# Kernel optimization log

Hardware: AMD Instinct MI355X
Metric: run time of the kernel (lower is better)

## Reference

```python
import jax, jax.numpy as jnp
import numpy as np
from jax import lax

B, C, H, W = 32, 64, 112, 112
ALPHA, BETA1, BETA2 = 0.25, 1.0, 1.0

# STE sign for weights (DifferntiableSign): fwd = +/-1, bwd mask |w|<=1 (w in [-1,1))
@jax.custom_vjp
def dsign(w):
    return jnp.where(w >= 0, 1.0, -1.0).astype(w.dtype)
def _dsign_fwd(w):
    return dsign(w), w
def _dsign_bwd(w, g):
    return (g * ((w < 1) & (w >= -1)).astype(g.dtype),)
dsign.defvjp(_dsign_fwd, _dsign_bwd)

# ReActNet BinaryActivation: fwd = sign(x), bwd piecewise-polynomial STE
@jax.custom_vjp
def bin_act(x):
    return jnp.where(x >= 0, 1.0, -1.0).astype(x.dtype)
def _ba_fwd(x):
    return bin_act(x), x
def _ba_bwd(x, g):
    slope = jnp.where((x >= -1) & (x < 0), 2.0 + 2.0 * x,
             jnp.where((x >= 0) & (x < 1), 2.0 - 2.0 * x, 0.0))
    return (g * slope.astype(g.dtype),)
bin_act.defvjp(_ba_fwd, _ba_bwd)

def scaled_sign_conv(x, w):
    # per-output-channel scale = mean(|w|) over (in, kh, kw)
    scale = jnp.mean(jnp.abs(w), axis=(1, 2, 3), keepdims=True)
    wb = scale * dsign(w)
    return lax.conv_general_dilated(x, wb, window_strides=(1, 1),
                                    padding=((1, 1), (1, 1)),
                                    dimension_numbers=("NCHW", "OIHW", "NCHW"))

def add_bias(x, b):
    return x + b[None, :, None, None]

def prelu(x, a):
    return jnp.where(x >= 0, x, a[None, :, None, None] * x)

def setup_inputs() -> dict:
    key = jax.random.key(0)
    ks = jax.random.split(key, 12)
    x = jax.random.normal(ks[0], (B, C, H, W), dtype=jnp.float32)
    # conv weights: symmetric uniform in [-1e-3, 1e-3] so signs are nontrivial
    w3 = (jax.random.uniform(ks[1], (C, C, 3, 3)) - 0.5) * 0.002
    w_pw = (jax.random.uniform(ks[2], (C, C, 3, 3)) - 0.5) * 0.002
    b11 = jax.random.normal(ks[3], (C,)) * 0.01
    b12 = jax.random.normal(ks[4], (C,)) * 0.01
    b13 = jax.random.normal(ks[5], (C,)) * 0.01
    b21 = jax.random.normal(ks[6], (C,)) * 0.01
    b22 = jax.random.normal(ks[7], (C,)) * 0.01
    b23 = jax.random.normal(ks[8], (C,)) * 0.01
    a1 = jax.random.uniform(ks[9], (C,), minval=0.1, maxval=0.4)
    a2 = jax.random.uniform(ks[10], (C,), minval=0.1, maxval=0.4)
    return {"x": x, "w3": w3, "w_pw": w_pw, "b11": b11, "b12": b12, "b13": b13,
            "b21": b21, "b22": b22, "b23": b23, "a1": a1, "a2": a2}

def reference(x, w3, w_pw, b11, b12, b13, b21, b22, b23, a1, a2):
    x_in = x * BETA1
    out1 = add_bias(x_in, b11)            # move11
    out1 = bin_act(out1)
    out1 = scaled_sign_conv(out1, w3)     # binary_3x3
    out1 = x + out1 * ALPHA               # stride==1: residual is original x
    out1 = add_bias(out1, b12)            # move12
    out1 = prelu(out1, a1)
    out1 = add_bias(out1, b13)            # move13
    out1_in = out1 * BETA2
    out2 = add_bias(out1_in, b21)         # move21
    out2 = bin_act(out2)
    out2 = scaled_sign_conv(out2, w_pw)   # binary_pw (3x3 per given defaults)
    out2 = out2 * ALPHA + out1
    out2 = add_bias(out2, b22)            # move22
    out2 = prelu(out2, a2)
    out2 = add_bias(out2, b23)            # move23
    return out2
```

## Files before the change

### kernel.cpp

```cpp
#include <hip/hip_runtime.h>
#include <hip/hip_fp16.h>
#include <stdint.h>

#define Bn 32
#define Cc 64
#define Hh 112
#define Ww 112
#define HWp (Hh*Ww)
#define NPIX (Bn*HWp)
#define PW 114
#define PHW (PW*PW)
#define NPAIR (HWp/2)
#define WROW (Ww/2)
#define ALPHA 0.25f
#define CSP 4
#define CPB (Cc/CSP)

typedef float    f32x2 __attribute__((ext_vector_type(2)));
typedef _Float16 f16x2 __attribute__((ext_vector_type(2)));

#define WB1_OFF   0
#define WB2_OFF   4608
#define ASC1_OFF  9216
#define ASC2_OFF  9472
#define CI1_OFF   9728
#define CI2_OFF   12288
#define BITS1_OFF 16384
#define BITS2_OFF (16384 + 3326976)
#define OUT1H_OFF (16384 + 2*3326976)
#define WS_NEED   (OUT1H_OFF + (size_t)NPIX*Cc*2)

#define MEMFENCE() asm volatile("" ::: "memory")

__global__ __launch_bounds__(64) void prep_weights(
        const float* __restrict__ w3, const float* __restrict__ wpw,
        uint64_t* __restrict__ wb1, uint64_t* __restrict__ wb2,
        float* __restrict__ asc1, float* __restrict__ asc2,
        int* __restrict__ ci1, int* __restrict__ ci2) {
    int b = blockIdx.x;
    int lane = threadIdx.x;
    const float* w  = (b < 64) ? w3   : wpw;
    uint64_t* wbits = (b < 64) ? wb1  : wb2;
    float*    ascp  = (b < 64) ? asc1 : asc2;
    int*      cip   = (b < 64) ? ci1  : ci2;
    int o = b & 63;
    const float* wp = w + ((size_t)o * Cc + lane) * 9;
    float v[9]; float asum = 0.f;
    #pragma unroll
    for (int t = 0; t < 9; ++t) { v[t] = wp[t]; asum += fabsf(v[t]); }
    uint64_t bal[9];
    #pragma unroll
    for (int t = 0; t < 9; ++t) bal[t] = __ballot(v[t] < 0.f);
    if (lane < 9) {
        wbits[o * 9 + lane] = bal[lane];
        int ty = lane, tr = ty / 3, tc = ty % 3;
        int sum = 0;
        #pragma unroll
        for (int t = 0; t < 9; ++t) {
            int r = t / 3, c = t % 3;
            bool inv = (tr == 0 && r == 0) || (tr == 2 && r == 2) ||
                       (tc == 0 && c == 0) || (tc == 2 && c == 2);
            if (inv) sum += 64 - 2 * (int)__popcll(bal[t]);
        }
        cip[o * 10 + ty] = 576 - sum;
    }
    #pragma unroll
    for (int off = 32; off > 0; off >>= 1) asum += __shfl_down(asum, off, 64);
    if (lane == 0) ascp[o] = ALPHA * asum * (1.f / 576.f);
}

__global__ __launch_bounds__(256, 4) void pack1(const float* __restrict__ x,
                                                const float* __restrict__ b11,
                                                uint64_t* __restrict__ bits1,
                                                uint64_t* __restrict__ bits2) {
    int n = blockIdx.y;
    int z = blockIdx.z;
    if (blockIdx.x >= 25) {
        if (z) return;
        int t = (blockIdx.x - 25) * 256 + threadIdx.x;
        if (t < 2 * PW + 2 * Hh) {
            int cell;
            if      (t < PW)          cell = t;
            else if (t < 2 * PW)      cell = 113 * PW + (t - PW);
            else if (t < 2 * PW + Hh) cell = (t - 2 * PW + 1) * PW;
            else                      cell = (t - 2 * PW - Hh + 1) * PW + 113;
            size_t bi = (size_t)n * PHW + cell;
            bits1[bi] = 0; bits2[bi] = 0;
        }
        return;
    }
    int p = blockIdx.x * 256 + threadIdx.x;
    if (p >= NPAIR) return;
    int h = p / WROW, w0 = (p - h * WROW) * 2;
    int hw = h * Ww + w0;
    int cb = z * 32;
    const float* xp = x + ((size_t)n * Cc + cb) * HWp + hw;
    size_t bi = (size_t)n * PHW + (h + 1) * PW + (w0 + 1);

    f32x2 v[32];
    #pragma unroll
    for (int j = 0; j < 32; ++j) v[j] = *(const f32x2*)(xp + (size_t)j * HWp);
    MEMFENCE();

    uint32_t ma = 0, mb = 0;
    #pragma unroll
    for (int j = 0; j < 32; ++j) {
        float bb = b11[cb + j];
        if (v[j].x + bb < 0.f) ma |= (1u << j);
        if (v[j].y + bb < 0.f) mb |= (1u << j);
    }
    uint32_t* wp1 = (uint32_t*)(bits1 + bi);
    wp1[z]     = ma;
    wp1[2 + z] = mb;
}

template <typename OutT>
__global__ __launch_bounds__(256, 4) void conv1_ep(
        const float* __restrict__ x, const uint64_t* __restrict__ bits1,
        const uint64_t* __restrict__ wb, const float* __restrict__ asc,
        const int* __restrict__ cint,
        const float* __restrict__ b12, const float* __restrict__ a1,
        const float* __restrict__ b13, const float* __restrict__ b21,
        OutT* __restrict__ out1, uint64_t* __restrict__ bits2) {
    __shared__ int lci[CPB * 10];
    int zb = blockIdx.z;
    int ob = zb * CPB;
    for (int i = threadIdx.x; i < CPB * 10; i += 256) lci[i] = cint[ob * 10 + i];
    __syncthreads();

    int p = blockIdx.x * 256 + threadIdx.x;
    if (p >= NPAIR) return;
    int n = blockIdx.y;
    int h = p / WROW, w0 = (p - h * WROW) * 2;
    int hw = h * Ww + w0;
    int rowp = (h == 0) ? 0 : (h == Hh - 1) ? 6 : 3;
    int t9a = rowp + ((w0 == 0) ? 0 : 1);
    int t9b = rowp + ((w0 + 1 == Ww - 1) ? 2 : 1);

    const uint64_t* bp = bits1 + (size_t)n * PHW + (h + 1) * PW + (w0 + 1);
    uint64_t q0[4], q1[4], q2[4];
    #pragma unroll
    for (int c = 0; c < 4; ++c) {
        q0[c] = bp[-PW - 1 + c]; q1[c] = bp[-1 + c]; q2[c] = bp[PW - 1 + c];
    }

    const float* xp = x + ((size_t)n * Cc + ob) * HWp + hw;
    OutT* op = out1 + ((size_t)n * Cc + ob) * HWp + hw;

    f32x2 cur[CPB];
    #pragma unroll
    for (int j = 0; j < CPB; ++j) cur[j] = *(const f32x2*)(xp + (size_t)j * HWp);
    MEMFENCE();

    uint32_t m2a = 0, m2b = 0;
    #pragma unroll
    for (int j = 0; j < CPB; ++j) {
        int o = ob + j;
        const uint64_t* wo = wb + o * 9;
        uint64_t t0 = wo[0], t1 = wo[1], t2 = wo[2], t3 = wo[3], t4 = wo[4],
                 t5 = wo[5], t6 = wo[6], t7 = wo[7], t8 = wo[8];
        int sa = (int)__popcll(q0[0] ^ t0) + (int)__popcll(q0[1] ^ t1) + (int)__popcll(q0[2] ^ t2)
               + (int)__popcll(q1[0] ^ t3) + (int)__popcll(q1[1] ^ t4) + (int)__popcll(q1[2] ^ t5)
               + (int)__popcll(q2[0] ^ t6) + (int)__popcll(q2[1] ^ t7) + (int)__popcll(q2[2] ^ t8);
        int sb = (int)__popcll(q0[1] ^ t0) + (int)__popcll(q0[2] ^ t1) + (int)__popcll(q0[3] ^ t2)
               + (int)__popcll(q1[1] ^ t3) + (int)__popcll(q1[2] ^ t4) + (int)__popcll(q1[3] ^ t5)
               + (int)__popcll(q2[1] ^ t6) + (int)__popcll(q2[2] ^ t7) + (int)__popcll(q2[3] ^ t8);
        int ca = lci[j * 10 + t9a];
        int cb = lci[j * 10 + t9b];
        float sc = asc[o], B2 = b12[o], Am1 = a1[o] - 1.0f, B3 = b13[o], B1 = b21[o];
        float va = fmaf(sc, (float)(ca - 2 * sa), cur[j].x);
        float vb = fmaf(sc, (float)(cb - 2 * sb), cur[j].y);
        va += B2; va = fmaf(fminf(va, 0.f), Am1, va); va += B3;
        vb += B2; vb = fmaf(fminf(vb, 0.f), Am1, vb); vb += B3;
        if constexpr (sizeof(OutT) == 2) {
            f16x2 hv; hv.x = (_Float16)va; hv.y = (_Float16)vb;
            *(f16x2*)(op + (size_t)j * HWp) = hv;
        } else {
            f32x2 fv; fv.x = va; fv.y = vb;
            *(f32x2*)(op + (size_t)j * HWp) = fv;
        }
        if (va + B1 < 0.f) m2a |= (1u << j);
        if (vb + B1 < 0.f) m2b |= (1u << j);
    }
    uint16_t* b2p = (uint16_t*)(bits2 + (size_t)n * PHW + (h + 1) * PW + (w0 + 1));
    b2p[zb]     = (uint16_t)m2a;
    b2p[4 + zb] = (uint16_t)m2b;
}

template <typename InT>
__global__ __launch_bounds__(256, 4) void conv2_ep(
        const uint64_t* __restrict__ bits2, const InT* __restrict__ out1,
        const uint64_t* __restrict__ wb, const float* __restrict__ asc,
        const int* __restrict__ cint,
        const float* __restrict__ b22, const float* __restrict__ a2,
        const float* __restrict__ b23, float* __restrict__ out) {
    __shared__ int lci[CPB * 10];
    int zb = blockIdx.z;
    int ob = zb * CPB;
    for (int i = threadIdx.x; i < CPB * 10; i += 256) lci[i] = cint[ob * 10 + i];
    __syncthreads();

    int p = blockIdx.x * 256 + threadIdx.x;
    if (p >= NPAIR) return;
    int n = blockIdx.y;
    int h = p / WROW, w0 = (p - h * WROW) * 2;
    int hw = h * Ww + w0;
    int rowp = (h == 0) ? 0 : (h == Hh - 1) ? 6 : 3;
    int t9a = rowp + ((w0 == 0) ? 0 : 1);
    int t9b = rowp + ((w0 + 1 == Ww - 1) ? 2 : 1);

    const uint64_t* bp = bits2 + (size_t)n * PHW + (h + 1) * PW + (w0 + 1);
    uint64_t q0[4], q1[4], q2[4];
    #pragma unroll
    for (int c = 0; c < 4; ++c) {
        q0[c] = bp[-PW - 1 + c]; q1[c] = bp[-1 + c]; q2[c] = bp[PW - 1 + c];
    }

    const InT* ip = out1 + ((size_t)n * Cc + ob) * HWp + hw;
    float* op = out + ((size_t)n * Cc + ob) * HWp + hw;

    f16x2 curh[CPB];
    f32x2 curf[CPB];
    if constexpr (sizeof(InT) == 2) {
        #pragma unroll
        for (int j = 0; j < CPB; ++j) curh[j] = *(const f16x2*)(ip + (size_t)j * HWp);
    } else {
        #pragma unroll
        for (int j = 0; j < CPB; ++j) curf[j] = *(const f32x2*)(ip + (size_t)j * HWp);
    }
    MEMFENCE();

    #pragma unroll
    for (int j = 0; j < CPB; ++j) {
        int o = ob + j;
        const uint64_t* wo = wb + o * 9;
        uint64_t t0 = wo[0], t1 = wo[1], t2 = wo[2], t3 = wo[3], t4 = wo[4],
                 t5 = wo[5], t6 = wo[6], t7 = wo[7], t8 = wo[8];
        int sa = (int)__popcll(q0[0] ^ t0) + (int)__popcll(q0[1] ^ t1) + (int)__popcll(q0[2] ^ t2)
               + (int)__popcll(q1[0] ^ t3) + (int)__popcll(q1[1] ^ t4) + (int)__popcll(q1[2] ^ t5)
               + (int)__popcll(q2[0] ^ t6) + (int)__popcll(q2[1] ^ t7) + (int)__popcll(q2[2] ^ t8);
        int sb = (int)__popcll(q0[1] ^ t0) + (int)__popcll(q0[2] ^ t1) + (int)__popcll(q0[3] ^ t2)
               + (int)__popcll(q1[1] ^ t3) + (int)__popcll(q1[2] ^ t4) + (int)__popcll(q1[3] ^ t5)
               + (int)__popcll(q2[1] ^ t6) + (int)__popcll(q2[2] ^ t7) + (int)__popcll(q2[3] ^ t8);
        int ca = lci[j * 10 + t9a];
        int cb = lci[j * 10 + t9b];
        float ra, rb;
        if constexpr (sizeof(InT) == 2) { ra = (float)curh[j].x; rb = (float)curh[j].y; }
        else                            { ra = curf[j].x;        rb = curf[j].y; }
        float sc = asc[o], B2 = b22[o], Am1 = a2[o] - 1.0f, B3 = b23[o];
        float va = fmaf(sc, (float)(ca - 2 * sa), ra);
        float vb = fmaf(sc, (float)(cb - 2 * sb), rb);
        va += B2; va = fmaf(fminf(va, 0.f), Am1, va); va += B3;
        vb += B2; vb = fmaf(fminf(vb, 0.f), Am1, vb); vb += B3;
        f32x2 fv; fv.x = va; fv.y = vb;
        __builtin_nontemporal_store(fv, (f32x2*)(op + (size_t)j * HWp));
    }
}

extern "C" void kernel_launch(void* const* d_in, const int* in_sizes, int n_in,
                              void* d_out, int out_size, void* d_ws, size_t ws_size,
                              hipStream_t stream) {
    const float* x    = (const float*)d_in[0];
    const float* w3   = (const float*)d_in[1];
    const float* wpw  = (const float*)d_in[2];
    const float* b11  = (const float*)d_in[3];
    const float* b12  = (const float*)d_in[4];
    const float* b13  = (const float*)d_in[5];
    const float* b21  = (const float*)d_in[6];
    const float* b22  = (const float*)d_in[7];
    const float* b23  = (const float*)d_in[8];
    const float* a1   = (const float*)d_in[9];
    const float* a2   = (const float*)d_in[10];

    char* ws = (char*)d_ws;
    uint64_t* wb1   = (uint64_t*)(ws + WB1_OFF);
    uint64_t* wb2   = (uint64_t*)(ws + WB2_OFF);
    float*    asc1  = (float*)(ws + ASC1_OFF);
    float*    asc2  = (float*)(ws + ASC2_OFF);
    int*      ci1   = (int*)(ws + CI1_OFF);
    int*      ci2   = (int*)(ws + CI2_OFF);
    uint64_t* bits1 = (uint64_t*)(ws + BITS1_OFF);
    uint64_t* bits2 = (uint64_t*)(ws + BITS2_OFF);
    float*    out   = (float*)d_out;

    dim3 pgrid(27, Bn, 2);
    dim3 cgrid((NPAIR + 255) / 256, Bn, CSP);

    prep_weights<<<128, 64, 0, stream>>>(w3, wpw, wb1, wb2, asc1, asc2, ci1, ci2);
    pack1<<<pgrid, 256, 0, stream>>>(x, b11, bits1, bits2);

    if (ws_size >= WS_NEED) {
        __half* out1h = (__half*)(ws + OUT1H_OFF);
        conv1_ep<__half><<<cgrid, 256, 0, stream>>>(x, bits1, wb1, asc1, ci1,
                                                    b12, a1, b13, b21, out1h, bits2);
        conv2_ep<__half><<<cgrid, 256, 0, stream>>>(bits2, out1h, wb2, asc2, ci2,
                                                    b22, a2, b23, out);
    } else {
        conv1_ep<float><<<cgrid, 256, 0, stream>>>(x, bits1, wb1, asc1, ci1,
                                                   b12, a1, b13, b21, out, bits2);
        conv2_ep<float><<<cgrid, 256, 0, stream>>>(bits2, out, wb2, asc2, ci2,
                                                   b22, a2, b23, out);
    }
}
```

Measured before the change: 272.2 us.

## Process four pixels per thread and split channels finer across blocks

Each thread in the pack and conv kernels now handles four adjacent pixels with 128-bit vector loads and stores instead of two. The channel split grows from 4 to 8 groups in the conv kernels and from 2 to 4 in the pack kernel, and the bit-mask writes shrink to 16-bit and 8-bit pieces. This reuses the loaded neighbour bit-words across more outputs and widens memory transactions, cutting redundant bit loads per pixel. In exchange each thread needs more registers, and the narrower partial writes into shared 64-bit words become finer-grained.

After: 271.6 us. No clear change (-0.2%).

```diff
diff --git a/kernel.cpp b/kernel.cpp
--- a/kernel.cpp
+++ b/kernel.cpp
@@ -10,14 +10,17 @@
 #define NPIX (Bn*HWp)
 #define PW 114
 #define PHW (PW*PW)
-#define NPAIR (HWp/2)
-#define WROW (Ww/2)
+#define NQUAD (HWp/4)
+#define QROW (Ww/4)
 #define ALPHA 0.25f
-#define CSP 4
-#define CPB (Cc/CSP)
+#define CSPC 8
+#define CPB (Cc/CSPC)
+#define PSP 4
 
 typedef float    f32x2 __attribute__((ext_vector_type(2)));
+typedef float    f32x4 __attribute__((ext_vector_type(4)));
 typedef _Float16 f16x2 __attribute__((ext_vector_type(2)));
+typedef _Float16 f16x4 __attribute__((ext_vector_type(4)));
 
 #define WB1_OFF   0
 #define WB2_OFF   4608
@@ -75,9 +78,9 @@
                                                 uint64_t* __restrict__ bits2) {
     int n = blockIdx.y;
     int z = blockIdx.z;
-    if (blockIdx.x >= 25) {
+    if (blockIdx.x >= 13) {
         if (z) return;
-        int t = (blockIdx.x - 25) * 256 + threadIdx.x;
+        int t = (blockIdx.x - 13) * 256 + threadIdx.x;
         if (t < 2 * PW + 2 * Hh) {
             int cell;
             if      (t < PW)          cell = t;
@@ -90,28 +93,33 @@
         return;
     }
     int p = blockIdx.x * 256 + threadIdx.x;
-    if (p >= NPAIR) return;
-    int h = p / WROW, w0 = (p - h * WROW) * 2;
+    if (p >= NQUAD) return;
+    int h = p / QROW, qx = p - h * QROW;
+    int w0 = qx * 4;
     int hw = h * Ww + w0;
-    int cb = z * 32;
+    int cb = z * 16;
     const float* xp = x + ((size_t)n * Cc + cb) * HWp + hw;
     size_t bi = (size_t)n * PHW + (h + 1) * PW + (w0 + 1);
 
-    f32x2 v[32];
-    #pragma unroll
-    for (int j = 0; j < 32; ++j) v[j] = *(const f32x2*)(xp + (size_t)j * HWp);
+    f32x4 v[16];
+    #pragma unroll
+    for (int j = 0; j < 16; ++j) v[j] = *(const f32x4*)(xp + (size_t)j * HWp);
     MEMFENCE();
 
-    uint32_t ma = 0, mb = 0;
-    #pragma unroll
-    for (int j = 0; j < 32; ++j) {
+    uint32_t ma = 0, mb = 0, mc = 0, md = 0;
+    #pragma unroll
+    for (int j = 0; j < 16; ++j) {
         float bb = b11[cb + j];
         if (v[j].x + bb < 0.f) ma |= (1u << j);
         if (v[j].y + bb < 0.f) mb |= (1u << j);
-    }
-    uint32_t* wp1 = (uint32_t*)(bits1 + bi);
-    wp1[z]     = ma;
-    wp1[2 + z] = mb;
+        if (v[j].z + bb < 0.f) mc |= (1u << j);
+        if (v[j].w + bb < 0.f) md |= (1u << j);
+    }
+    uint16_t* wp1 = (uint16_t*)(bits1 + bi);
+    wp1[z]      = (uint16_t)ma;
+    wp1[4 + z]  = (uint16_t)mb;
+    wp1[8 + z]  = (uint16_t)mc;
+    wp1[12 + z] = (uint16_t)md;
 }
 
 template <typename OutT>
@@ -129,30 +137,32 @@
     __syncthreads();
 
     int p = blockIdx.x * 256 + threadIdx.x;
-    if (p >= NPAIR) return;
+    if (p >= NQUAD) return;
     int n = blockIdx.y;
-    int h = p / WROW, w0 = (p - h * WROW) * 2;
+    int h = p / QROW, qx = p - h * QROW;
+    int w0 = qx * 4;
     int hw = h * Ww + w0;
     int rowp = (h == 0) ? 0 : (h == Hh - 1) ? 6 : 3;
-    int t9a = rowp + ((w0 == 0) ? 0 : 1);
-    int t9b = rowp + ((w0 + 1 == Ww - 1) ? 2 : 1);
+    int t9a = rowp + ((qx == 0) ? 0 : 1);
+    int t9m = rowp + 1;
+    int t9d = rowp + ((qx == QROW - 1) ? 2 : 1);
 
     const uint64_t* bp = bits1 + (size_t)n * PHW + (h + 1) * PW + (w0 + 1);
-    uint64_t q0[4], q1[4], q2[4];
-    #pragma unroll
-    for (int c = 0; c < 4; ++c) {
+    uint64_t q0[6], q1[6], q2[6];
+    #pragma unroll
+    for (int c = 0; c < 6; ++c) {
         q0[c] = bp[-PW - 1 + c]; q1[c] = bp[-1 + c]; q2[c] = bp[PW - 1 + c];
     }
 
     const float* xp = x + ((size_t)n * Cc + ob) * HWp + hw;
     OutT* op = out1 + ((size_t)n * Cc + ob) * HWp + hw;
 
-    f32x2 cur[CPB];
-    #pragma unroll
-    for (int j = 0; j < CPB; ++j) cur[j] = *(const f32x2*)(xp + (size_t)j * HWp);
+    f32x4 cur[CPB];
+    #pragma unroll
+    for (int j = 0; j < CPB; ++j) cur[j] = *(const f32x4*)(xp + (size_t)j * HWp);
     MEMFENCE();
 
-    uint32_t m2a = 0, m2b = 0;
+    uint32_t m2a = 0, m2b = 0, m2c = 0, m2d = 0;
     #pragma unroll
     for (int j = 0; j < CPB; ++j) {
         int o = ob + j;
@@ -165,26 +175,42 @@
         int sb = (int)__popcll(q0[1] ^ t0) + (int)__popcll(q0[2] ^ t1) + (int)__popcll(q0[3] ^ t2)
                + (int)__popcll(q1[1] ^ t3) + (int)__popcll(q1[2] ^ t4) + (int)__popcll(q1[3] ^ t5)
                + (int)__popcll(q2[1] ^ t6) + (int)__popcll(q2[2] ^ t7) + (int)__popcll(q2[3] ^ t8);
+        int sc_ = (int)__popcll(q0[2] ^ t0) + (int)__popcll(q0[3] ^ t1) + (int)__popcll(q0[4] ^ t2)
+               + (int)__popcll(q1[2] ^ t3) + (int)__popcll(q1[3] ^ t4) + (int)__popcll(q1[4] ^ t5)
+               + (int)__popcll(q2[2] ^ t6) + (int)__popcll(q2[3] ^ t7) + (int)__popcll(q2[4] ^ t8);
+        int sd = (int)__popcll(q0[3] ^ t0) + (int)__popcll(q0[4] ^ t1) + (int)__popcll(q0[5] ^ t2)
+               + (int)__popcll(q1[3] ^ t3) + (int)__popcll(q1[4] ^ t4) + (int)__popcll(q1[5] ^ t5)
+               + (int)__popcll(q2[3] ^ t6) + (int)__popcll(q2[4] ^ t7) + (int)__popcll(q2[5] ^ t8);
         int ca = lci[j * 10 + t9a];
-        int cb = lci[j * 10 + t9b];
-        float sc = asc[o], B2 = b12[o], Am1 = a1[o] - 1.0f, B3 = b13[o], B1 = b21[o];
-        float va = fmaf(sc, (float)(ca - 2 * sa), cur[j].x);
-        float vb = fmaf(sc, (float)(cb - 2 * sb), cur[j].y);
+        int cm = lci[j * 10 + t9m];
+        int cd = lci[j * 10 + t9d];
+        float scl = asc[o], B2 = b12[o], Am1 = a1[o] - 1.0f, B3 = b13[o], B1 = b21[o];
+        float va = fmaf(scl, (float)(ca - 2 * sa), cur[j].x);
+        float vb = fmaf(scl, (float)(cm - 2 * sb), cur[j].y);
+        float vc = fmaf(scl, (float)(cm - 2 * sc_), cur[j].z);
+        float vd = fmaf(scl, (float)(cd - 2 * sd), cur[j].w);
         va += B2; va = fmaf(fminf(va, 0.f), Am1, va); va += B3;
         vb += B2; vb = fmaf(fminf(vb, 0.f), Am1, vb); vb += B3;
+        vc += B2; vc = fmaf(fminf(vc, 0.f), Am1, vc); vc += B3;
+        vd += B2; vd = fmaf(fminf(vd, 0.f), Am1, vd); vd += B3;
         if constexpr (sizeof(OutT) == 2) {
-            f16x2 hv; hv.x = (_Float16)va; hv.y = (_Float16)vb;
-            *(f16x2*)(op + (size_t)j * HWp) = hv;
+            f16x4 hv; hv.x = (_Float16)va; hv.y = (_Float16)vb;
+            hv.z = (_Float16)vc; hv.w = (_Float16)vd;
+            *(f16x4*)(op + (size_t)j * HWp) = hv;
         } else {
-            f32x2 fv; fv.x = va; fv.y = vb;
-            *(f32x2*)(op + (size_t)j * HWp) = fv;
+            f32x4 fv; fv.x = va; fv.y = vb; fv.z = vc; fv.w = vd;
+            *(f32x4*)(op + (size_t)j * HWp) = fv;
         }
         if (va + B1 < 0.f) m2a |= (1u << j);
         if (vb + B1 < 0.f) m2b |= (1u << j);
-    }
-    uint16_t* b2p = (uint16_t*)(bits2 + (size_t)n * PHW + (h + 1) * PW + (w0 + 1));
-    b2p[zb]     = (uint16_t)m2a;
-    b2p[4 + zb] = (uint16_t)m2b;
+        if (vc + B1 < 0.f) m2c |= (1u << j);
+        if (vd + B1 < 0.f) m2d |= (1u << j);
+    }
+    uint8_t* b2p = (uint8_t*)(bits2 + (size_t)n * PHW + (h + 1) * PW + (w0 + 1));
+    b2p[zb]      = (uint8_t)m2a;
+    b2p[8 + zb]  = (uint8_t)m2b;
+    b2p[16 + zb] = (uint8_t)m2c;
+    b2p[24 + zb] = (uint8_t)m2d;
 }
 
 template <typename InT>
@@ -201,32 +227,34 @@
     __syncthreads();
 
     int p = blockIdx.x * 256 + threadIdx.x;
-    if (p >= NPAIR) return;
+    if (p >= NQUAD) return;
     int n = blockIdx.y;
-    int h = p / WROW, w0 = (p - h * WROW) * 2;
+    int h = p / QROW, qx = p - h * QROW;
+    int w0 = qx * 4;
     int hw = h * Ww + w0;
     int rowp = (h == 0) ? 0 : (h == Hh - 1) ? 6 : 3;
-    int t9a = rowp + ((w0 == 0) ? 0 : 1);
-    int t9b = rowp + ((w0 + 1 == Ww - 1) ? 2 : 1);
+    int t9a = rowp + ((qx == 0) ? 0 : 1);
+    int t9m = rowp + 1;
+    int t9d = rowp + ((qx == QROW - 1) ? 2 : 1);
 
     const uint64_t* bp = bits2 + (size_t)n * PHW + (h + 1) * PW + (w0 + 1);
-    uint64_t q0[4], q1[4], q2[4];
-    #pragma unroll
-    for (int c = 0; c < 4; ++c) {
+    uint64_t q0[6], q1[6], q2[6];
+    #pragma unroll
+    for (int c = 0; c < 6; ++c) {
         q0[c] = bp[-PW - 1 + c]; q1[c] = bp[-1 + c]; q2[c] = bp[PW - 1 + c];
     }
 
     const InT* ip = out1 + ((size_t)n * Cc + ob) * HWp + hw;
     float* op = out + ((size_t)n * Cc + ob) * HWp + hw;
 
-    f16x2 curh[CPB];
-    f32x2 curf[CPB];
+    f16x4 curh[CPB];
+    f32x4 curf[CPB];
     if constexpr (sizeof(InT) == 2) {
         #pragma unroll
-        for (int j = 0; j < CPB; ++j) curh[j] = *(const f16x2*)(ip + (size_t)j * HWp);
+        for (int j = 0; j < CPB; ++j) curh[j] = *(const f16x4*)(ip + (size_t)j * HWp);
     } else {
         #pragma unroll
-        for (int j = 0; j < CPB; ++j) curf[j] = *(const f32x2*)(ip + (size_t)j * HWp);
+        for (int j = 0; j < CPB; ++j) curf[j] = *(const f32x4*)(ip + (size_t)j * HWp);
     }
     MEMFENCE();
 
@@ -242,18 +270,33 @@
         int sb = (int)__popcll(q0[1] ^ t0) + (int)__popcll(q0[2] ^ t1) + (int)__popcll(q0[3] ^ t2)
                + (int)__popcll(q1[1] ^ t3) + (int)__popcll(q1[2] ^ t4) + (int)__popcll(q1[3] ^ t5)
                + (int)__popcll(q2[1] ^ t6) + (int)__popcll(q2[2] ^ t7) + (int)__popcll(q2[3] ^ t8);
+        int sc_ = (int)__popcll(q0[2] ^ t0) + (int)__popcll(q0[3] ^ t1) + (int)__popcll(q0[4] ^ t2)
+               + (int)__popcll(q1[2] ^ t3) + (int)__popcll(q1[3] ^ t4) + (int)__popcll(q1[4] ^ t5)
+               + (int)__popcll(q2[2] ^ t6) + (int)__popcll(q2[3] ^ t7) + (int)__popcll(q2[4] ^ t8);
+        int sd = (int)__popcll(q0[3] ^ t0) + (int)__popcll(q0[4] ^ t1) + (int)__popcll(q0[5] ^ t2)
+               + (int)__popcll(q1[3] ^ t3) + (int)__popcll(q1[4] ^ t4) + (int)__popcll(q1[5] ^ t5)
+               + (int)__popcll(q2[3] ^ t6) + (int)__popcll(q2[4] ^ t7) + (int)__popcll(q2[5] ^ t8);
         int ca = lci[j * 10 + t9a];
-        int cb = lci[j * 10 + t9b];
-        float ra, rb;
-        if constexpr (sizeof(InT) == 2) { ra = (float)curh[j].x; rb = (float)curh[j].y; }
-        else                            { ra = curf[j].x;        rb = curf[j].y; }
-        float sc = asc[o], B2 = b22[o], Am1 = a2[o] - 1.0f, B3 = b23[o];
-        float va = fmaf(sc, (float)(ca - 2 * sa), ra);
-        float vb = fmaf(sc, (float)(cb - 2 * sb), rb);
+        int cm = lci[j * 10 + t9m];
+        int cd = lci[j * 10 + t9d];
+        float ra, rb, rc, rd;
+        if constexpr (sizeof(InT) == 2) {
+            ra = (float)curh[j].x; rb = (float)curh[j].y;
+            rc = (float)curh[j].z; rd = (float)curh[j].w;
+        } else {
+            ra = curf[j].x; rb = curf[j].y; rc = curf[j].z; rd = curf[j].w;
+        }
+        float scl = asc[o], B2 = b22[o], Am1 = a2[o] - 1.0f, B3 = b23[o];
+        float va = fmaf(scl, (float)(ca - 2 * sa), ra);
+        float vb = fmaf(scl, (float)(cm - 2 * sb), rb);
+        float vc = fmaf(scl, (float)(cm - 2 * sc_), rc);
+        float vd = fmaf(scl, (float)(cd - 2 * sd), rd);
         va += B2; va = fmaf(fminf(va, 0.f), Am1, va); va += B3;
         vb += B2; vb = fmaf(fminf(vb, 0.f), Am1, vb); vb += B3;
-        f32x2 fv; fv.x = va; fv.y = vb;
-        __builtin_nontemporal_store(fv, (f32x2*)(op + (size_t)j * HWp));
+        vc += B2; vc = fmaf(fminf(vc, 0.f), Am1, vc); vc += B3;
+        vd += B2; vd = fmaf(fminf(vd, 0.f), Am1, vd); vd += B3;
+        f32x4 fv; fv.x = va; fv.y = vb; fv.z = vc; fv.w = vd;
+        __builtin_nontemporal_store(fv, (f32x4*)(op + (size_t)j * HWp));
     }
 }
 
@@ -283,8 +326,8 @@
     uint64_t* bits2 = (uint64_t*)(ws + BITS2_OFF);
     float*    out   = (float*)d_out;
 
-    dim3 pgrid(27, Bn, 2);
-    dim3 cgrid((NPAIR + 255) / 256, Bn, CSP);
+    dim3 pgrid(15, Bn, PSP);
+    dim3 cgrid((NQUAD + 255) / 256, Bn, CSPC);
 
     prep_weights<<<128, 64, 0, stream>>>(w3, wpw, wb1, wb2, asc1, asc2, ci1, ci2);
     pack1<<<pgrid, 256, 0, stream>>>(x, b11, bits1, bits2);
```
